# Performance work log

Hardware: AMD Instinct MI355X
Metric: run time of the kernel (lower is better)

Reference implementation:

```python
import jax, jax.numpy as jnp
import numpy as np

N_ATOMS = 100000
M_NBR = 12
ORIG_FEA = 92
NBR_FEA = 41
AF = 64          # atom_fea_len
N_CONV = 3
OUT_DIM = 128
N_CRYSTALS = 2000
ATOMS_PER = 50
EPS = 1e-5


def setup_inputs() -> dict:
    key = jax.random.key(0)
    ks = jax.random.split(key, 12)
    inp = {
        "atom_fea": jax.random.normal(ks[0], (N_ATOMS, ORIG_FEA), dtype=jnp.float32),
        "nbr_fea": jax.random.normal(ks[1], (N_ATOMS, M_NBR, NBR_FEA), dtype=jnp.float32),
        "nbr_fea_idx": jax.random.randint(ks[2], (N_ATOMS, M_NBR), 0, N_ATOMS, dtype=jnp.int32),
        "crystal_atom_idx": jnp.arange(N_CRYSTALS * ATOMS_PER, dtype=jnp.int32).reshape(N_CRYSTALS, ATOMS_PER),
    }
    # parameters
    inp["W_embed"] = jax.random.normal(ks[3], (ORIG_FEA, AF), dtype=jnp.float32) * 0.05
    inp["b_embed"] = jnp.zeros((AF,), dtype=jnp.float32)
    in_full = 2 * AF + NBR_FEA  # 169
    inp["W_full"] = jax.random.normal(ks[4], (N_CONV, in_full, 2 * AF), dtype=jnp.float32) * 0.05
    inp["b_full"] = jnp.zeros((N_CONV, 2 * AF), dtype=jnp.float32)
    inp["bn1_gamma"] = jnp.ones((N_CONV, 2 * AF), dtype=jnp.float32)
    inp["bn1_beta"] = jnp.zeros((N_CONV, 2 * AF), dtype=jnp.float32)
    inp["bn2_gamma"] = jnp.ones((N_CONV, AF), dtype=jnp.float32)
    inp["bn2_beta"] = jnp.zeros((N_CONV, AF), dtype=jnp.float32)
    inp["W_pool"] = jax.random.normal(ks[5], (AF, OUT_DIM), dtype=jnp.float32) * 0.05
    inp["b_pool"] = jnp.zeros((OUT_DIM,), dtype=jnp.float32)
    return inp


def _batchnorm(x, gamma, beta):
    # training-mode BatchNorm1d over leading dim, biased variance
    m = jnp.mean(x, axis=0)
    v = jnp.var(x, axis=0)
    return (x - m) * jax.lax.rsqrt(v + EPS) * gamma + beta


def _conv_layer(x, nbr_fea, nbr_fea_idx, Wf, bf, g1, be1, g2, be2):
    N, M = nbr_fea_idx.shape
    nbr_atom = x[nbr_fea_idx]                                  # [N, M, AF] gather
    self_fea = jnp.broadcast_to(x[:, None, :], (N, M, AF))     # [N, M, AF]
    total = jnp.concatenate([self_fea, nbr_atom, nbr_fea], axis=2)  # [N, M, 2AF+NBR]
    gated = jnp.einsum('nmi,io->nmo', total, Wf) + bf          # [N, M, 2AF]
    gated = _batchnorm(gated.reshape(N * M, 2 * AF), g1, be1).reshape(N, M, 2 * AF)
    nbr_filter = jax.nn.sigmoid(gated[..., :AF])
    nbr_core = jax.nn.softplus(gated[..., AF:])
    nbr_sumed = jnp.sum(nbr_filter * nbr_core, axis=1)         # [N, AF]
    nbr_sumed = _batchnorm(nbr_sumed, g2, be2)
    return jax.nn.softplus(x + nbr_sumed)


def reference(atom_fea, nbr_fea, nbr_fea_idx, crystal_atom_idx,
              W_embed, b_embed, W_full, b_full,
              bn1_gamma, bn1_beta, bn2_gamma, bn2_beta,
              W_pool, b_pool):
    x = atom_fea @ W_embed + b_embed                           # [N, AF]
    for i in range(N_CONV):
        x = _conv_layer(x, nbr_fea, nbr_fea_idx,
                        W_full[i], b_full[i],
                        bn1_gamma[i], bn1_beta[i],
                        bn2_gamma[i], bn2_beta[i])
    crystal_fea = jnp.mean(x[crystal_atom_idx], axis=1)        # [G, AF] per-graph mean pool
    return jax.nn.relu(crystal_fea @ W_pool + b_pool)          # [G, OUT_DIM]
```

## Files before the change

kernel.cpp:

```cpp
#include <hip/hip_runtime.h>
#include <hip/hip_fp16.h>
#include <math.h>

#define N_ATOMS 100000
#define M_NBR 12
#define ORIG_FEA 92
#define NBR_FEA 41
#define AF 64
#define OUT2 128
#define IN_FULL 169
#define N_CONV 3
#define OUT_DIM 128
#define N_CRYSTALS 2000
#define ATOMS_PER 50
#define EPS 1e-5f

#define ZCH 16
#define EDGES (ZCH * M_NBR)
#define NF_STRIDE 44
#define YB_ATOMS 80
#define YB_CHUNK 16

typedef _Float16 h4 __attribute__((ext_vector_type(4)));

__device__ __forceinline__ float softplus_f(float x) {
    return fmaxf(x, 0.0f) + __logf(1.0f + __expf(-fabsf(x)));
}
__device__ __forceinline__ float sigmoid_f(float x) {
    return __builtin_amdgcn_rcpf(1.0f + __expf(-x));
}
__device__ __forceinline__ void fma4(float4& a, float s, const float4& b) {
    a.x = fmaf(s, b.x, a.x); a.y = fmaf(s, b.y, a.y);
    a.z = fmaf(s, b.z, a.z); a.w = fmaf(s, b.w, a.w);
}
__device__ __forceinline__ float4 zero4() { return make_float4(0.f, 0.f, 0.f, 0.f); }

union H4 { uint2 u; __half2 h[2]; };
__device__ __forceinline__ void store_h4(__half* p, float4 v) {
    H4 t;
    t.h[0] = __floats2half2_rn(v.x, v.y);
    t.h[1] = __floats2half2_rn(v.z, v.w);
    *(uint2*)p = t.u;
}
__device__ __forceinline__ float4 load_h4(const __half* p) {
    H4 t; t.u = *(const uint2*)p;
    float2 a = __half22float2(t.h[0]);
    float2 b = __half22float2(t.h[1]);
    return make_float4(a.x, a.y, b.x, b.y);
}

__global__ __launch_bounds__(256, 2) void k_embed(
    const float* __restrict__ af, const float* __restrict__ W,
    const float* __restrict__ b, float* __restrict__ x) {
  __shared__ __align__(16) float saf[64 * ORIG_FEA];
  int a0 = blockIdx.x * 64;
  int na = min(64, N_ATOMS - a0);
  int tid = threadIdx.x;
  int c = tid & 63, rgrp = tid >> 6;
  float w[ORIG_FEA];
#pragma unroll
  for (int k = 0; k < ORIG_FEA; ++k) w[k] = W[k * AF + c];
  int n4 = na * (ORIG_FEA / 4);
  const float4* g4 = (const float4*)(af + (size_t)a0 * ORIG_FEA);
  float4* s4 = (float4*)saf;
  for (int e = tid; e < n4; e += 256) s4[e] = g4[e];
  __syncthreads();
  float bc = b[c];
  for (int a = rgrp; a < na; a += 4) {
    float acc = bc;
    const float4* row = (const float4*)(saf + a * ORIG_FEA);
#pragma unroll
    for (int q = 0; q < ORIG_FEA / 4; ++q) {
      float4 v = row[q];
      acc = fmaf(v.x, w[4 * q], acc);
      acc = fmaf(v.y, w[4 * q + 1], acc);
      acc = fmaf(v.z, w[4 * q + 2], acc);
      acc = fmaf(v.w, w[4 * q + 3], acc);
    }
    x[(size_t)(a0 + a) * AF + c] = acc;
  }
}

__global__ __launch_bounds__(256, 2) void k_ysn(
    const float* __restrict__ x, const float* __restrict__ Wf,
    float* __restrict__ y_self, float* __restrict__ y_nbr) {
  __shared__ __align__(16) float sW2[64 * 256];
  __shared__ __align__(16) float sx[YB_CHUNK * AF];
  int tid = threadIdx.x;
  int cg = tid & 31, ag = tid >> 5;
  int c0 = cg * 4;
  {
    float4* s4 = (float4*)sW2;
    const float4* g4 = (const float4*)Wf;
    for (int e = tid; e < 64 * 64; e += 256) {
      int r = e >> 6, q = e & 63;
      s4[r * 64 + q] = (q < 32) ? g4[r * 32 + q] : g4[(64 + r) * 32 + (q - 32)];
    }
  }
  int ab = blockIdx.x * YB_ATOMS;
  for (int cc = 0; cc < YB_ATOMS / YB_CHUNK; ++cc) {
    int a0 = ab + cc * YB_CHUNK;
    __syncthreads();
    {
      float4* s4 = (float4*)sx;
      const float4* g4 = (const float4*)(x + (size_t)a0 * AF);
      for (int e = tid; e < YB_CHUNK * AF / 4; e += 256) s4[e] = g4[e];
    }
    __syncthreads();
    float4 accs[2] = {zero4(), zero4()};
    float4 accn[2] = {zero4(), zero4()};
    for (int k0 = 0; k0 < AF; k0 += 4) {
      float4 av0 = *(const float4*)(sx + (ag * 2 + 0) * AF + k0);
      float4 av1 = *(const float4*)(sx + (ag * 2 + 1) * AF + k0);
#pragma unroll
      for (int kk = 0; kk < 4; ++kk) {
        float4 b0 = *(const float4*)(sW2 + (k0 + kk) * 256 + c0);
        float4 b1 = *(const float4*)(sW2 + (k0 + kk) * 256 + 128 + c0);
        float s0 = (kk == 0) ? av0.x : (kk == 1) ? av0.y : (kk == 2) ? av0.z : av0.w;
        float s1 = (kk == 0) ? av1.x : (kk == 1) ? av1.y : (kk == 2) ? av1.z : av1.w;
        fma4(accs[0], s0, b0); fma4(accn[0], s0, b1);
        fma4(accs[1], s1, b0); fma4(accn[1], s1, b1);
      }
    }
#pragma unroll
    for (int t = 0; t < 2; ++t) {
      size_t n = (size_t)(a0 + ag * 2 + t);
      *(float4*)(y_self + n * OUT2 + c0) = accs[t];
      *(float4*)(y_nbr + n * OUT2 + c0) = accn[t];
    }
  }
}

__device__ __forceinline__ void edge_gemm(
    const _Float16* snf, const float* sW, int ebase, int c0,
    float4 acc0[6], float4 acc1[6]) {
#pragma unroll
  for (int e = 0; e < 6; ++e) { acc0[e] = zero4(); acc1[e] = zero4(); }
  for (int k0 = 0; k0 < 40; k0 += 4) {
    h4 av[6];
#pragma unroll
    for (int e = 0; e < 6; ++e)
      av[e] = *(const h4*)(snf + (ebase + e) * NF_STRIDE + k0);
#pragma unroll
    for (int kk = 0; kk < 4; ++kk) {
      float4 b0 = *(const float4*)(sW + (k0 + kk) * OUT2 + c0);
      float4 b1 = *(const float4*)(sW + (k0 + kk) * OUT2 + AF + c0);
#pragma unroll
      for (int e = 0; e < 6; ++e) {
        float s = (float)av[e][kk];
        fma4(acc0[e], s, b0);
        fma4(acc1[e], s, b1);
      }
    }
  }
  {
    float4 b0 = *(const float4*)(sW + 40 * OUT2 + c0);
    float4 b1 = *(const float4*)(sW + 40 * OUT2 + AF + c0);
#pragma unroll
    for (int e = 0; e < 6; ++e) {
      float s = (float)snf[(ebase + e) * NF_STRIDE + 40];
      fma4(acc0[e], s, b0);
      fma4(acc1[e], s, b1);
    }
  }
}

__device__ __forceinline__ void stage_edge(
    const float* __restrict__ nbr_fea, const int* __restrict__ nidx,
    const float* __restrict__ We, int a0, int tid,
    _Float16* snf, float* sW, int* sidx) {
  float4* sW4 = (float4*)sW;
  const float4* gW4 = (const float4*)We;
  for (int e = tid; e < NBR_FEA * (OUT2 / 4); e += 256) sW4[e] = gW4[e];
  const float* gnf = nbr_fea + (size_t)a0 * M_NBR * NBR_FEA;
  for (int e = tid; e < EDGES * NBR_FEA; e += 256) {
    int r = e / NBR_FEA;
    int k = e - r * NBR_FEA;
    snf[r * NF_STRIDE + k] = (_Float16)gnf[e];
  }
  for (int e = tid; e < EDGES; e += 256) {
    snf[e * NF_STRIDE + 41] = (_Float16)0.f;
    snf[e * NF_STRIDE + 42] = (_Float16)0.f;
    snf[e * NF_STRIDE + 43] = (_Float16)0.f;
    sidx[e] = nidx[(size_t)a0 * M_NBR + e];
  }
}

template <int WZ>
__global__ __launch_bounds__(256, 2) void k_zstats_t(
    const float* __restrict__ nbr_fea, const int* __restrict__ nidx,
    const float* __restrict__ y_self, const float* __restrict__ y_nbr,
    const float* __restrict__ Wf, const float* __restrict__ bf,
    float* __restrict__ gsum, float* __restrict__ gsumsq,
    __half* __restrict__ z16) {
  __shared__ __align__(16) _Float16 snf[EDGES * NF_STRIDE];
  __shared__ __align__(16) float sW[NBR_FEA * OUT2];
  __shared__ int sidx[EDGES];
  __shared__ float lsum[OUT2], lsumsq[OUT2];
  int tid = threadIdx.x;
  int cg = tid & 15, eg = tid >> 4;
  int c0 = cg * 4;
  if (tid < OUT2) { lsum[tid] = 0.f; lsumsq[tid] = 0.f; }
  int a0 = blockIdx.x * ZCH;
  stage_edge(nbr_fea, nidx, Wf + 2 * AF * OUT2, a0, tid, snf, sW, sidx);
  __syncthreads();
  float4 bz0 = *(const float4*)(bf + c0);
  float4 bz1 = *(const float4*)(bf + AF + c0);
  float4 sm0 = zero4(), sq0 = zero4(), sm1 = zero4(), sq1 = zero4();
  for (int c = 0; c < 2; ++c) {
    int ebase = c * 96 + eg * 6;
    int atomL = c * 8 + (eg >> 1);
    const float* ys = y_self + (size_t)(a0 + atomL) * OUT2;
    float4 y0 = *(const float4*)(ys + c0);
    float4 y1 = *(const float4*)(ys + AF + c0);
    float4 acc0[6], acc1[6];
    edge_gemm(snf, sW, ebase, c0, acc0, acc1);
#pragma unroll
    for (int e = 0; e < 6; ++e) {
      int j = sidx[ebase + e];
      const float* yn = y_nbr + (size_t)j * OUT2;
      float4 n0 = *(const float4*)(yn + c0);
      float4 n1 = *(const float4*)(yn + AF + c0);
      float4 z0, z1;
      z0.x = acc0[e].x + y0.x + n0.x + bz0.x; z0.y = acc0[e].y + y0.y + n0.y + bz0.y;
      z0.z = acc0[e].z + y0.z + n0.z + bz0.z; z0.w = acc0[e].w + y0.w + n0.w + bz0.w;
      z1.x = acc1[e].x + y1.x + n1.x + bz1.x; z1.y = acc1[e].y + y1.y + n1.y + bz1.y;
      z1.z = acc1[e].z + y1.z + n1.z + bz1.z; z1.w = acc1[e].w + y1.w + n1.w + bz1.w;
      if (WZ) {
        __half* zp = z16 + ((size_t)a0 * M_NBR + ebase + e) * OUT2 + c0;
        store_h4(zp, z0);
        store_h4(zp + AF, z1);
      }
      sm0.x += z0.x; sm0.y += z0.y; sm0.z += z0.z; sm0.w += z0.w;
      sm1.x += z1.x; sm1.y += z1.y; sm1.z += z1.z; sm1.w += z1.w;
      sq0.x = fmaf(z0.x, z0.x, sq0.x); sq0.y = fmaf(z0.y, z0.y, sq0.y);
      sq0.z = fmaf(z0.z, z0.z, sq0.z); sq0.w = fmaf(z0.w, z0.w, sq0.w);
      sq1.x = fmaf(z1.x, z1.x, sq1.x); sq1.y = fmaf(z1.y, z1.y, sq1.y);
      sq1.z = fmaf(z1.z, z1.z, sq1.z); sq1.w = fmaf(z1.w, z1.w, sq1.w);
    }
  }
  atomicAdd(&lsum[c0 + 0], sm0.x); atomicAdd(&lsum[c0 + 1], sm0.y);
  atomicAdd(&lsum[c0 + 2], sm0.z); atomicAdd(&lsum[c0 + 3], sm0.w);
  atomicAdd(&lsum[AF + c0 + 0], sm1.x); atomicAdd(&lsum[AF + c0 + 1], sm1.y);
  atomicAdd(&lsum[AF + c0 + 2], sm1.z); atomicAdd(&lsum[AF + c0 + 3], sm1.w);
  atomicAdd(&lsumsq[c0 + 0], sq0.x); atomicAdd(&lsumsq[c0 + 1], sq0.y);
  atomicAdd(&lsumsq[c0 + 2], sq0.z); atomicAdd(&lsumsq[c0 + 3], sq0.w);
  atomicAdd(&lsumsq[AF + c0 + 0], sq1.x); atomicAdd(&lsumsq[AF + c0 + 1], sq1.y);
  atomicAdd(&lsumsq[AF + c0 + 2], sq1.z); atomicAdd(&lsumsq[AF + c0 + 3], sq1.w);
  __syncthreads();
  if (tid < OUT2) {
    atomicAdd(&gsum[tid], lsum[tid]);
    atomicAdd(&gsumsq[tid], lsumsq[tid]);
  }
}

__global__ __launch_bounds__(256, 4) void k_apply_stream(
    const __half* __restrict__ z16,
    const float* __restrict__ sc1, const float* __restrict__ sh1,
    float* __restrict__ s_out, float* __restrict__ gsum, float* __restrict__ gsumsq) {
  __shared__ float lsum[AF], lsumsq[AF];
  int tid = threadIdx.x;
  if (tid < AF) { lsum[tid] = 0.f; lsumsq[tid] = 0.f; }
  __syncthreads();
  int cg = tid & 15, a = tid >> 4;
  int c0 = cg * 4;
  size_t atom = (size_t)blockIdx.x * 16 + a;
  float4 f0 = *(const float4*)(sc1 + c0);
  float4 g0 = *(const float4*)(sh1 + c0);
  float4 f1 = *(const float4*)(sc1 + AF + c0);
  float4 g1 = *(const float4*)(sh1 + AF + c0);
  const __half* zr = z16 + atom * (M_NBR * OUT2);
  float4 sacc = zero4();
#pragma unroll 4
  for (int m = 0; m < M_NBR; ++m) {
    float4 zf = load_h4(zr + m * OUT2 + c0);
    float4 zc = load_h4(zr + m * OUT2 + AF + c0);
    zf.x = fmaf(zf.x, f0.x, g0.x); zf.y = fmaf(zf.y, f0.y, g0.y);
    zf.z = fmaf(zf.z, f0.z, g0.z); zf.w = fmaf(zf.w, f0.w, g0.w);
    zc.x = fmaf(zc.x, f1.x, g1.x); zc.y = fmaf(zc.y, f1.y, g1.y);
    zc.z = fmaf(zc.z, f1.z, g1.z); zc.w = fmaf(zc.w, f1.w, g1.w);
    sacc.x = fmaf(sigmoid_f(zf.x), softplus_f(zc.x), sacc.x);
    sacc.y = fmaf(sigmoid_f(zf.y), softplus_f(zc.y), sacc.y);
    sacc.z = fmaf(sigmoid_f(zf.z), softplus_f(zc.z), sacc.z);
    sacc.w = fmaf(sigmoid_f(zf.w), softplus_f(zc.w), sacc.w);
  }
  *(float4*)(s_out + atom * AF + c0) = sacc;
  float4 sq;
  sq.x = sacc.x * sacc.x; sq.y = sacc.y * sacc.y;
  sq.z = sacc.z * sacc.z; sq.w = sacc.w * sacc.w;
  sacc.x += __shfl_xor(sacc.x, 16, 64); sacc.y += __shfl_xor(sacc.y, 16, 64);
  sacc.z += __shfl_xor(sacc.z, 16, 64); sacc.w += __shfl_xor(sacc.w, 16, 64);
  sq.x += __shfl_xor(sq.x, 16, 64); sq.y += __shfl_xor(sq.y, 16, 64);
  sq.z += __shfl_xor(sq.z, 16, 64); sq.w += __shfl_xor(sq.w, 16, 64);
  sacc.x += __shfl_xor(sacc.x, 32, 64); sacc.y += __shfl_xor(sacc.y, 32, 64);
  sacc.z += __shfl_xor(sacc.z, 32, 64); sacc.w += __shfl_xor(sacc.w, 32, 64);
  sq.x += __shfl_xor(sq.x, 32, 64); sq.y += __shfl_xor(sq.y, 32, 64);
  sq.z += __shfl_xor(sq.z, 32, 64); sq.w += __shfl_xor(sq.w, 32, 64);
  if ((tid & 48) == 0) {
    atomicAdd(&lsum[c0 + 0], sacc.x); atomicAdd(&lsum[c0 + 1], sacc.y);
    atomicAdd(&lsum[c0 + 2], sacc.z); atomicAdd(&lsum[c0 + 3], sacc.w);
    atomicAdd(&lsumsq[c0 + 0], sq.x); atomicAdd(&lsumsq[c0 + 1], sq.y);
    atomicAdd(&lsumsq[c0 + 2], sq.z); atomicAdd(&lsumsq[c0 + 3], sq.w);
  }
  __syncthreads();
  if (tid < AF) {
    atomicAdd(&gsum[tid], lsum[tid]);
    atomicAdd(&gsumsq[tid], lsumsq[tid]);
  }
}

__global__ __launch_bounds__(256, 2) void k_apply(
    const float* __restrict__ nbr_fea, const int* __restrict__ nidx,
    const float* __restrict__ y_self, const float* __restrict__ y_nbr,
    const float* __restrict__ Wf, const float* __restrict__ bf,
    const float* __restrict__ sc1, const float* __restrict__ sh1,
    float* __restrict__ s_out, float* __restrict__ gsum, float* __restrict__ gsumsq) {
  __shared__ __align__(16) _Float16 snf[EDGES * NF_STRIDE];
  __shared__ __align__(16) float sW[NBR_FEA * OUT2];
  __shared__ int sidx[EDGES];
  __shared__ float lsum[AF], lsumsq[AF];
  int tid = threadIdx.x;
  int cg = tid & 15, eg = tid >> 4;
  int c0 = cg * 4;
  if (tid < AF) { lsum[tid] = 0.f; lsumsq[tid] = 0.f; }
  int a0 = blockIdx.x * ZCH;
  stage_edge(nbr_fea, nidx, Wf + 2 * AF * OUT2, a0, tid, snf, sW, sidx);
  __syncthreads();
  float4 bz0 = *(const float4*)(bf + c0);
  float4 bz1 = *(const float4*)(bf + AF + c0);
  float4 f0 = *(const float4*)(sc1 + c0);
  float4 g0 = *(const float4*)(sh1 + c0);
  float4 f1 = *(const float4*)(sc1 + AF + c0);
  float4 g1 = *(const float4*)(sh1 + AF + c0);
  for (int c = 0; c < 2; ++c) {
    int ebase = c * 96 + eg * 6;
    int atomL = c * 8 + (eg >> 1);
    const float* ys = y_self + (size_t)(a0 + atomL) * OUT2;
    float4 y0 = *(const float4*)(ys + c0);
    float4 y1 = *(const float4*)(ys + AF + c0);
    float4 acc0[6], acc1[6];
    edge_gemm(snf, sW, ebase, c0, acc0, acc1);
    float4 sacc = zero4();
#pragma unroll
    for (int e = 0; e < 6; ++e) {
      int j = sidx[ebase + e];
      const float* yn = y_nbr + (size_t)j * OUT2;
      float4 n0 = *(const float4*)(yn + c0);
      float4 n1 = *(const float4*)(yn + AF + c0);
      float4 z0, z1;
      z0.x = fmaf(acc0[e].x + y0.x + n0.x + bz0.x, f0.x, g0.x);
      z0.y = fmaf(acc0[e].y + y0.y + n0.y + bz0.y, f0.y, g0.y);
      z0.z = fmaf(acc0[e].z + y0.z + n0.z + bz0.z, f0.z, g0.z);
      z0.w = fmaf(acc0[e].w + y0.w + n0.w + bz0.w, f0.w, g0.w);
      z1.x = fmaf(acc1[e].x + y1.x + n1.x + bz1.x, f1.x, g1.x);
      z1.y = fmaf(acc1[e].y + y1.y + n1.y + bz1.y, f1.y, g1.y);
      z1.z = fmaf(acc1[e].z + y1.z + n1.z + bz1.z, f1.z, g1.z);
      z1.w = fmaf(acc1[e].w + y1.w + n1.w + bz1.w, f1.w, g1.w);
      sacc.x = fmaf(sigmoid_f(z0.x), softplus_f(z1.x), sacc.x);
      sacc.y = fmaf(sigmoid_f(z0.y), softplus_f(z1.y), sacc.y);
      sacc.z = fmaf(sigmoid_f(z0.z), softplus_f(z1.z), sacc.z);
      sacc.w = fmaf(sigmoid_f(z0.w), softplus_f(z1.w), sacc.w);
    }
    sacc.x += __shfl_xor(sacc.x, 16, 64);
    sacc.y += __shfl_xor(sacc.y, 16, 64);
    sacc.z += __shfl_xor(sacc.z, 16, 64);
    sacc.w += __shfl_xor(sacc.w, 16, 64);
    if ((eg & 1) == 0) {
      *(float4*)(s_out + (size_t)(a0 + atomL) * AF + c0) = sacc;
      atomicAdd(&lsum[c0 + 0], sacc.x); atomicAdd(&lsum[c0 + 1], sacc.y);
      atomicAdd(&lsum[c0 + 2], sacc.z); atomicAdd(&lsum[c0 + 3], sacc.w);
      atomicAdd(&lsumsq[c0 + 0], sacc.x * sacc.x);
      atomicAdd(&lsumsq[c0 + 1], sacc.y * sacc.y);
      atomicAdd(&lsumsq[c0 + 2], sacc.z * sacc.z);
      atomicAdd(&lsumsq[c0 + 3], sacc.w * sacc.w);
    }
  }
  __syncthreads();
  if (tid < AF) {
    atomicAdd(&gsum[tid], lsum[tid]);
    atomicAdd(&gsumsq[tid], lsumsq[tid]);
  }
}

__global__ void k_finalize(const float* __restrict__ gsum, const float* __restrict__ gsumsq,
                           const float* __restrict__ gamma, const float* __restrict__ beta,
                           float* __restrict__ scale, float* __restrict__ shift,
                           int chn, float invcount) {
  int c = threadIdx.x;
  if (c < chn) {
    float m = gsum[c] * invcount;
    float v = gsumsq[c] * invcount - m * m;
    float sc = gamma[c] * rsqrtf(v + EPS);
    scale[c] = sc;
    shift[c] = beta[c] - m * sc;
  }
}

__global__ __launch_bounds__(256) void k_update(
    float* __restrict__ x, const float* __restrict__ s,
    const float* __restrict__ sc2, const float* __restrict__ sh2) {
  int e = blockIdx.x * 256 + threadIdx.x;
  if (e < N_ATOMS * AF) {
    int c = e & (AF - 1);
    float v = x[e] + s[e] * sc2[c] + sh2[c];
    x[e] = softplus_f(v);
  }
}

__global__ __launch_bounds__(128) void k_pool(
    const float* __restrict__ x, const int* __restrict__ cidx,
    const float* __restrict__ Wp, const float* __restrict__ bp,
    float* __restrict__ out) {
  __shared__ float part[2][AF];
  __shared__ float mean[AF];
  int g = blockIdx.x, tid = threadIdx.x;
  int c = tid & 63, h = tid >> 6;
  float acc = 0.f;
  for (int a = h; a < ATOMS_PER; a += 2) {
    int idx = cidx[g * ATOMS_PER + a];
    acc += x[(size_t)idx * AF + c];
  }
  part[h][c] = acc;
  __syncthreads();
  if (tid < AF) mean[tid] = (part[0][tid] + part[1][tid]) * (1.0f / ATOMS_PER);
  __syncthreads();
  float o = bp[tid];
#pragma unroll
  for (int k = 0; k < AF; ++k) o += mean[k] * Wp[k * OUT_DIM + tid];
  out[(size_t)g * OUT_DIM + tid] = fmaxf(o, 0.f);
}

extern "C" void kernel_launch(void* const* d_in, const int* in_sizes, int n_in,
                              void* d_out, int out_size, void* d_ws, size_t ws_size,
                              hipStream_t stream) {
  const float* atom_fea = (const float*)d_in[0];
  const float* nbr_fea  = (const float*)d_in[1];
  const int*   nbr_idx  = (const int*)d_in[2];
  const int*   cidx     = (const int*)d_in[3];
  const float* W_embed  = (const float*)d_in[4];
  const float* b_embed  = (const float*)d_in[5];
  const float* W_full   = (const float*)d_in[6];
  const float* b_full   = (const float*)d_in[7];
  const float* bn1_g    = (const float*)d_in[8];
  const float* bn1_b    = (const float*)d_in[9];
  const float* bn2_g    = (const float*)d_in[10];
  const float* bn2_b    = (const float*)d_in[11];
  const float* W_pool   = (const float*)d_in[12];
  const float* b_pool   = (const float*)d_in[13];
  float* out = (float*)d_out;

  float* ws = (float*)d_ws;
  size_t off = 0;
  float* x      = ws + off; off += (size_t)N_ATOMS * AF;
  float* y_self = ws + off; off += (size_t)N_ATOMS * OUT2;
  float* y_nbr  = ws + off; off += (size_t)N_ATOMS * OUT2;
  float* s_buf  = ws + off; off += (size_t)N_ATOMS * AF;
  float* sums   = ws + off; off += (size_t)N_CONV * 384;
  float* affine = ws + off; off += (size_t)N_CONV * 384;

  size_t base_bytes = (off * sizeof(float) + 255) & ~(size_t)255;
  size_t z_bytes = (size_t)N_ATOMS * M_NBR * OUT2 * sizeof(__half);
  bool fast = ws_size >= base_bytes + z_bytes;
  __half* z16 = fast ? (__half*)((char*)d_ws + base_bytes) : nullptr;

  hipMemsetAsync(sums, 0, (size_t)N_CONV * 384 * sizeof(float), stream);

  k_embed<<<(N_ATOMS + 63) / 64, 256, 0, stream>>>(atom_fea, W_embed, b_embed, x);

  for (int i = 0; i < N_CONV; ++i) {
    const float* Wf = W_full + (size_t)i * IN_FULL * OUT2;
    const float* bf = b_full + (size_t)i * OUT2;
    float* sum1   = sums + (size_t)i * 384;
    float* sumsq1 = sum1 + OUT2;
    float* sum2   = sumsq1 + OUT2;
    float* sumsq2 = sum2 + AF;
    float* sc1 = affine + (size_t)i * 384;
    float* sh1 = sc1 + OUT2;
    float* sc2 = sh1 + OUT2;
    float* sh2 = sc2 + AF;

    k_ysn<<<N_ATOMS / YB_ATOMS, 256, 0, stream>>>(x, Wf, y_self, y_nbr);
    if (fast) {
      k_zstats_t<1><<<N_ATOMS / ZCH, 256, 0, stream>>>(
          nbr_fea, nbr_idx, y_self, y_nbr, Wf, bf, sum1, sumsq1, z16);
    } else {
      k_zstats_t<0><<<N_ATOMS / ZCH, 256, 0, stream>>>(
          nbr_fea, nbr_idx, y_self, y_nbr, Wf, bf, sum1, sumsq1, nullptr);
    }
    k_finalize<<<1, 128, 0, stream>>>(sum1, sumsq1, bn1_g + i * OUT2, bn1_b + i * OUT2,
                                      sc1, sh1, OUT2, 1.0f / ((float)N_ATOMS * M_NBR));
    if (fast) {
      k_apply_stream<<<N_ATOMS / 16, 256, 0, stream>>>(z16, sc1, sh1, s_buf,
                                                       sum2, sumsq2);
    } else {
      k_apply<<<N_ATOMS / ZCH, 256, 0, stream>>>(nbr_fea, nbr_idx, y_self, y_nbr,
                                                 Wf, bf, sc1, sh1, s_buf, sum2, sumsq2);
    }
    k_finalize<<<1, 128, 0, stream>>>(sum2, sumsq2, bn2_g + i * AF, bn2_b + i * AF,
                                      sc2, sh2, AF, 1.0f / (float)N_ATOMS);
    k_update<<<(N_ATOMS * AF + 255) / 256, 256, 0, stream>>>(x, s_buf, sc2, sh2);
  }

  k_pool<<<N_CRYSTALS, 128, 0, stream>>>(x, cidx, W_pool, b_pool, out);
}
```

Baseline: 2.190 ms.

## Replace LDS-tiled edge GEMM with wave-per-atom register-resident weight kernel

Adds a persistent kernel in which each wavefront processes one atom at a time, keeps the 41x2 edge-weight column slice in registers per lane, and reads nbr_fea directly as scalar, wave-uniform loads. This drops the LDS staging of nbr_fea and the weights, the fp16 conversion and the block barriers of the tiled kernel. The old tiled kernel is kept only for the non-fast path, with its z-store removed. The cost is about 82 registers per lane just for weights, full-precision FMAs without reuse of nbr_fea across columns, and a fixed grid of 1024 blocks.

```diff
diff --git a/kernel.cpp b/kernel.cpp
--- a/kernel.cpp
+++ b/kernel.cpp
@@ -20,6 +20,9 @@
 #define NF_STRIDE 44
 #define YB_ATOMS 80
 #define YB_CHUNK 16
+
+#define ZW_BLOCKS 1024
+#define ZW_WAVES (ZW_BLOCKS * 4)
 
 typedef _Float16 h4 __attribute__((ext_vector_type(4)));
 
@@ -131,6 +134,65 @@
   }
 }
 
+template <int WZ>
+__global__ __launch_bounds__(256, 3) void k_zstats_w(
+    const float* __restrict__ nbr_fea, const int* __restrict__ nidx,
+    const float* __restrict__ y_self, const float* __restrict__ y_nbr,
+    const float* __restrict__ Wf, const float* __restrict__ bf,
+    float* __restrict__ gsum, float* __restrict__ gsumsq,
+    __half* __restrict__ z16) {
+  __shared__ float lsum[OUT2], lsumsq[OUT2];
+  int tid = threadIdx.x;
+  int lane = tid & 63;
+  int wid = tid >> 6;
+  if (tid < OUT2) { lsum[tid] = 0.f; lsumsq[tid] = 0.f; }
+  __syncthreads();
+  const float* We = Wf + 2 * AF * OUT2;
+  int c2 = lane * 2;
+  float wlo[NBR_FEA], whi[NBR_FEA];
+#pragma unroll
+  for (int k = 0; k < NBR_FEA; ++k) {
+    float2 wv = *(const float2*)(We + k * OUT2 + c2);
+    wlo[k] = wv.x; whi[k] = wv.y;
+  }
+  float2 bv = *(const float2*)(bf + c2);
+  float slo = 0.f, shi = 0.f, qlo = 0.f, qhi = 0.f;
+  int w = __builtin_amdgcn_readfirstlane(blockIdx.x * 4 + wid);
+  for (int a = w; a < N_ATOMS; a += ZW_WAVES) {
+    float2 ys = *(const float2*)(y_self + (size_t)a * OUT2 + c2);
+    float blo = ys.x + bv.x, bhi = ys.y + bv.y;
+    const float* nfr = nbr_fea + (size_t)a * (M_NBR * NBR_FEA);
+    const int* idxr = nidx + (size_t)a * M_NBR;
+#pragma unroll 2
+    for (int m = 0; m < M_NBR; ++m) {
+      int j = idxr[m];
+      float2 yn = *(const float2*)(y_nbr + (size_t)j * OUT2 + c2);
+      float zlo = blo + yn.x, zhi = bhi + yn.y;
+      const float* nf = nfr + m * NBR_FEA;
+#pragma unroll
+      for (int k = 0; k < NBR_FEA; ++k) {
+        float s = nf[k];
+        zlo = fmaf(s, wlo[k], zlo);
+        zhi = fmaf(s, whi[k], zhi);
+      }
+      if (WZ) {
+        __half2 h = __floats2half2_rn(zlo, zhi);
+        *(__half2*)(z16 + ((size_t)a * M_NBR + m) * OUT2 + c2) = h;
+      }
+      slo += zlo; shi += zhi;
+      qlo = fmaf(zlo, zlo, qlo);
+      qhi = fmaf(zhi, zhi, qhi);
+    }
+  }
+  atomicAdd(&lsum[c2], slo);     atomicAdd(&lsum[c2 + 1], shi);
+  atomicAdd(&lsumsq[c2], qlo);   atomicAdd(&lsumsq[c2 + 1], qhi);
+  __syncthreads();
+  if (tid < OUT2) {
+    atomicAdd(&gsum[tid], lsum[tid]);
+    atomicAdd(&gsumsq[tid], lsumsq[tid]);
+  }
+}
+
 __device__ __forceinline__ void edge_gemm(
     const _Float16* snf, const float* sW, int ebase, int c0,
     float4 acc0[6], float4 acc1[6]) {
@@ -186,13 +248,11 @@
   }
 }
 
-template <int WZ>
-__global__ __launch_bounds__(256, 2) void k_zstats_t(
+__global__ __launch_bounds__(256, 2) void k_zstats_fb(
     const float* __restrict__ nbr_fea, const int* __restrict__ nidx,
     const float* __restrict__ y_self, const float* __restrict__ y_nbr,
     const float* __restrict__ Wf, const float* __restrict__ bf,
-    float* __restrict__ gsum, float* __restrict__ gsumsq,
-    __half* __restrict__ z16) {
+    float* __restrict__ gsum, float* __restrict__ gsumsq) {
   __shared__ __align__(16) _Float16 snf[EDGES * NF_STRIDE];
   __shared__ __align__(16) float sW[NBR_FEA * OUT2];
   __shared__ int sidx[EDGES];
@@ -226,11 +286,6 @@
       z0.z = acc0[e].z + y0.z + n0.z + bz0.z; z0.w = acc0[e].w + y0.w + n0.w + bz0.w;
       z1.x = acc1[e].x + y1.x + n1.x + bz1.x; z1.y = acc1[e].y + y1.y + n1.y + bz1.y;
       z1.z = acc1[e].z + y1.z + n1.z + bz1.z; z1.w = acc1[e].w + y1.w + n1.w + bz1.w;
-      if (WZ) {
-        __half* zp = z16 + ((size_t)a0 * M_NBR + ebase + e) * OUT2 + c0;
-        store_h4(zp, z0);
-        store_h4(zp + AF, z1);
-      }
       sm0.x += z0.x; sm0.y += z0.y; sm0.z += z0.z; sm0.w += z0.w;
       sm1.x += z1.x; sm1.y += z1.y; sm1.z += z1.z; sm1.w += z1.w;
       sq0.x = fmaf(z0.x, z0.x, sq0.x); sq0.y = fmaf(z0.y, z0.y, sq0.y);
@@ -481,11 +536,11 @@
 
     k_ysn<<<N_ATOMS / YB_ATOMS, 256, 0, stream>>>(x, Wf, y_self, y_nbr);
     if (fast) {
-      k_zstats_t<1><<<N_ATOMS / ZCH, 256, 0, stream>>>(
+      k_zstats_w<1><<<ZW_BLOCKS, 256, 0, stream>>>(
           nbr_fea, nbr_idx, y_self, y_nbr, Wf, bf, sum1, sumsq1, z16);
     } else {
-      k_zstats_t<0><<<N_ATOMS / ZCH, 256, 0, stream>>>(
-          nbr_fea, nbr_idx, y_self, y_nbr, Wf, bf, sum1, sumsq1, nullptr);
+      k_zstats_fb<<<N_ATOMS / ZCH, 256, 0, stream>>>(
+          nbr_fea, nbr_idx, y_self, y_nbr, Wf, bf, sum1, sumsq1);
     }
     k_finalize<<<1, 128, 0, stream>>>(sum1, sumsq1, bn1_g + i * OUT2, bn1_b + i * OUT2,
                                       sc1, sh1, OUT2, 1.0f / ((float)N_ATOMS * M_NBR));
```

Result: faster. 2.078 ms (-5.1%).
